# Kernel optimization log

Hardware: AMD Instinct MI355X
Metric: run time of the kernel (lower is better)

Reference implementation:

```python
import jax, jax.numpy as jnp
import numpy as np

B, T, N, U = 64, 128, 128, 128  # batch, seq_len, n_features, lstm units


def setup_inputs() -> dict:
    key = jax.random.key(0)
    ks = jax.random.split(key, 8)
    s = 0.05
    return {
        "x": jax.random.normal(ks[0], (B, T, N), dtype=jnp.float32),
        "hidden_state": jnp.zeros((B, U), jnp.float32),
        "cell_state": jnp.zeros((B, U), jnp.float32),
        "lstm_kernel": jax.random.normal(ks[1], (N, 4 * U), jnp.float32) * s,
        "lstm_bias": jnp.zeros((4 * U,), jnp.float32),
        "w1_kernel": jax.random.normal(ks[2], (1, T), jnp.float32) * s,
        "w1_bias": jnp.zeros((T,), jnp.float32),
        "w2_kernel": jax.random.normal(ks[3], (2 * U, T), jnp.float32) * s,
        "w2_bias": jnp.zeros((T,), jnp.float32),
        "v_kernel": jax.random.normal(ks[4], (T, 1), jnp.float32) * s,
        "v_bias": jnp.zeros((1,), jnp.float32),
        "n": N,
    }


def reference(x, hidden_state, cell_state, lstm_kernel, lstm_bias,
              w1_kernel, w1_bias, w2_kernel, w2_bias, v_kernel, v_bias, n):
    # NewLSTM ignores the provided initial state, so every timestep's LSTM
    # runs a length-1 sequence from zero (h, c). No recurrence -> vectorize
    # over time. Keras gate order: i, f, c(g), o; recurrent kernel * 0 drops out.
    z = x @ lstm_kernel + lstm_bias                       # (B,T,4U)
    i, f, g, o = jnp.split(z, 4, axis=-1)
    c = jax.nn.sigmoid(i) * jnp.tanh(g)                   # f-gate * c_prev(=0) vanishes
    h = jax.nn.sigmoid(o) * jnp.tanh(c)                   # (B,T,U)

    # Input attention per timestep, vectorized over T.
    query = jnp.concatenate([h, c], axis=-1)              # (B,T,2U)
    s2 = query @ w2_kernel + w2_bias                      # (B,T,T)
    # w1 is Dense(T) on a size-1 feature axis: x_scalar * w1_kernel[0] + b.
    s1 = x[..., None] * w1_kernel[0] + w1_bias            # (B,T,N,T)
    score = jnp.tanh(s1 + s2[:, :, None, :])              # (B,T,N,T)
    e = jnp.einsum('btnk,k->btn', score, v_kernel[:, 0]) + v_bias[0]  # (B,T,N)
    alpha = jax.nn.softmax(e, axis=-1)                    # softmax over features

    return x * alpha                                      # (B,T,N)
```

## Files before the change

kernel.cpp:

```cpp
#include <hip/hip_runtime.h>
#include <math.h>


typedef __attribute__((ext_vector_type(8))) short short8;
typedef __attribute__((ext_vector_type(4))) float f32x4;

#define BT 8192
#define NF 128
#define K_C     2.8853900817779268f
#define K_LOG2E 1.4426950408889634f

__device__ __forceinline__ float fast_rcp(float x)  { return __builtin_amdgcn_rcpf(x); }
__device__ __forceinline__ float fast_exp2(float x) { return __builtin_amdgcn_exp2f(x); }

__device__ __forceinline__ float tanh_nc(float tC) {
    return fmaf(-2.f, fast_rcp(1.f + fast_exp2(tC)), 1.f);
}
__device__ __forceinline__ float tanh_fast(float t) { return tanh_nc(t * K_C); }
__device__ __forceinline__ float sig_fast(float z) {
    return fast_rcp(1.f + fast_exp2(-K_LOG2E * z));
}
__device__ __forceinline__ unsigned short f2bf(float f) {
    unsigned u = __float_as_uint(f);
    return (unsigned short)((u + 0x7fffu + ((u >> 16) & 1u)) >> 16);
}

__global__ __launch_bounds__(64) void prep(const float* __restrict__ Wl,
                                           const float* __restrict__ w2,
                                           unsigned short* __restrict__ wsB) {
    const int lane = threadIdx.x;
    const int n16 = lane & 15, q = lane >> 4;
    const int b = blockIdx.x;
    if (b < 96) {
        const int nt = b >> 2, kk = b & 3;
        const int g = nt >> 3, jt = nt & 7;
        const int goff = (g == 0) ? 0 : (g == 1 ? 256 : 384);
        const int col = goff + jt * 16 + n16;
        unsigned short* d = wsB + b * 512 + lane * 8;
        #pragma unroll
        for (int j = 0; j < 8; j++)
            d[j] = f2bf(Wl[(kk * 32 + q * 8 + j) * 512 + col]);
    } else {
        const int fs = b - 96;
        const int nt2 = fs >> 3, kk2 = fs & 7;
        const int col = nt2 * 16 + n16;
        unsigned short* d = wsB + 49152 + fs * 512 + lane * 8;
        #pragma unroll
        for (int j = 0; j < 8; j++)
            d[j] = f2bf(w2[(kk2 * 32 + q * 8 + j) * 128 + col]);
    }
}

__global__ __launch_bounds__(256, 2) void enc(
    const float* __restrict__ x,  const unsigned short* __restrict__ wsB,
    const float* __restrict__ bl, const float* __restrict__ b2,
    const float* __restrict__ b1, const float* __restrict__ w1,
    const float* __restrict__ v,  float* __restrict__ out)
{
    __shared__ __align__(16) float xs[16][NF];
    __shared__ unsigned short Qf[8 * 512];
    __shared__ __align__(16) float c2[16][NF];
    __shared__ __align__(16) float w1Cs[NF], vs[NF];
    __shared__ float Ftab[16][32];
    __shared__ float rowMn[16], rowMx[16];

    const int t    = threadIdx.x;
    const int lane = t & 63, w = t >> 6;
    const int n16  = lane & 15, q = lane >> 4;
    const int rowbase = blockIdx.x * 16;

    for (int i = t; i < 512; i += 256)
        ((float4*)xs)[i] = ((const float4*)(x + rowbase * NF))[i];
    if (t < NF) { w1Cs[t] = w1[t] * K_C; vs[t] = v[t]; }

    short8 af[4];
    const float* xrow = x + (rowbase + n16) * NF + q * 8;
    #pragma unroll
    for (int kk = 0; kk < 4; kk++) {
        const float4 v0 = *(const float4*)(xrow + kk * 32);
        const float4 v1 = *(const float4*)(xrow + kk * 32 + 4);
        short8 a;
        a[0] = f2bf(v0.x); a[1] = f2bf(v0.y); a[2] = f2bf(v0.z); a[3] = f2bf(v0.w);
        a[4] = f2bf(v1.x); a[5] = f2bf(v1.y); a[6] = f2bf(v1.z); a[7] = f2bf(v1.w);
        af[kk] = a;
    }

    f32x4 acc[2][3];
    #pragma unroll
    for (int j2 = 0; j2 < 2; j2++)
        #pragma unroll
        for (int g = 0; g < 3; g++) acc[j2][g] = (f32x4)(0.f);
    const short8* B1g = (const short8*)wsB;
    #pragma unroll
    for (int kk = 0; kk < 4; kk++)
        #pragma unroll
        for (int j2 = 0; j2 < 2; j2++) {
            const int jt = w * 2 + j2;
            #pragma unroll
            for (int g = 0; g < 3; g++) {
                const short8 bf = B1g[(((g * 8 + jt) * 4) + kk) * 64 + lane];
                acc[j2][g] = __builtin_amdgcn_mfma_f32_16x16x32_bf16(
                    af[kk], bf, acc[j2][g], 0, 0, 0);
            }
        }

    #pragma unroll
    for (int j2 = 0; j2 < 2; j2++) {
        const int jt = w * 2 + j2;
        const int u  = jt * 16 + n16;
        const float bi = bl[u], bg = bl[256 + u], bo = bl[384 + u];
        const int kqh = u, kqc = NF + u;
        const int baseh = (kqh >> 5) * 512 + ((kqh & 31) >> 3) * 128 + q * 32 + (kqh & 7);
        const int basec = (kqc >> 5) * 512 + ((kqc & 31) >> 3) * 128 + q * 32 + (kqc & 7);
        #pragma unroll
        for (int r = 0; r < 4; r++) {
            const float c = sig_fast(acc[j2][0][r] + bi) * tanh_fast(acc[j2][1][r] + bg);
            const float h = sig_fast(acc[j2][2][r] + bo) * tanh_fast(c);
            Qf[baseh + r * 8] = f2bf(h);
            Qf[basec + r * 8] = f2bf(c);
        }
    }
    __syncthreads();

    short8 a2[8];
    #pragma unroll
    for (int kk2 = 0; kk2 < 8; kk2++)
        a2[kk2] = *(const short8*)&Qf[kk2 * 512 + lane * 8];
    const short8* B2g = (const short8*)(wsB + 49152);
    #pragma unroll
    for (int j2 = 0; j2 < 2; j2++) {
        const int nt2 = w * 2 + j2;
        f32x4 acc2 = (f32x4)(0.f);
        #pragma unroll
        for (int kk2 = 0; kk2 < 8; kk2++) {
            const short8 bf = B2g[(nt2 * 8 + kk2) * 64 + lane];
            acc2 = __builtin_amdgcn_mfma_f32_16x16x32_bf16(a2[kk2], bf, acc2, 0, 0, 0);
        }
        const int u2 = nt2 * 16 + n16;
        const float bias2 = (b2[u2] + b1[u2]) * K_C;
        #pragma unroll
        for (int r = 0; r < 4; r++)
            c2[q * 4 + r][u2] = fmaf(acc2[r], K_C, bias2);
    }

    #pragma unroll
    for (int r4 = 0; r4 < 4; r4++) {
        const int row = w * 4 + r4;
        float a = xs[row][lane], b = xs[row][64 + lane];
        float mn = fminf(a, b), mx = fmaxf(a, b);
        #pragma unroll
        for (int off = 1; off < 64; off <<= 1) {
            mn = fminf(mn, __shfl_xor(mn, off, 64));
            mx = fmaxf(mx, __shfl_xor(mx, off, 64));
        }
        if (lane == 0) { rowMn[row] = mn; rowMx[row] = mx; }
    }
    __syncthreads();

    #pragma unroll
    for (int p = 0; p < 2; p++) {
        const int row = p * 8 + (t >> 5);
        const int m   = t & 31;
        const float mn = rowMn[row];
        const float h  = (rowMx[row] - mn) * (1.f / 29.f);
        const float xi = fmaf((float)(m - 1), h, mn);
        float accF = 0.f;
        #pragma unroll 4
        for (int k = 0; k < NF; k += 4) {
            const float4 w4 = *(const float4*)&w1Cs[k];
            const float4 c4 = *(const float4*)&c2[row][k];
            const float4 v4 = *(const float4*)&vs[k];
            accF = fmaf(tanh_nc(fmaf(xi, w4.x, c4.x)), v4.x, accF);
            accF = fmaf(tanh_nc(fmaf(xi, w4.y, c4.y)), v4.y, accF);
            accF = fmaf(tanh_nc(fmaf(xi, w4.z, c4.z)), v4.z, accF);
            accF = fmaf(tanh_nc(fmaf(xi, w4.w, c4.w)), v4.w, accF);
        }
        Ftab[row][m] = accF;
    }
    __syncthreads();

    {
        const int row = t >> 4;
        const int n0  = (t & 15) * 8;
        const float mn   = rowMn[row];
        const float span = rowMx[row] - mn;
        const float invh = span > 1e-12f ? 29.f / span : 0.f;
        float xv[8], e8[8];
        *(float4*)&xv[0] = *(const float4*)&xs[row][n0];
        *(float4*)&xv[4] = *(const float4*)&xs[row][n0 + 4];
        #pragma unroll
        for (int i = 0; i < 8; i++) {
            const float sN = fmaf(xv[i] - mn, invh, 1.0f);
            int ii = (int)sN;
            ii = ii < 1 ? 1 : (ii > 29 ? 29 : ii);
            const float f  = sN - (float)ii;
            const float F0 = Ftab[row][ii - 1], F1 = Ftab[row][ii];
            const float F2 = Ftab[row][ii + 1], F3 = Ftab[row][ii + 2];
            e8[i] = F1 + 0.5f * f * ((F2 - F0)
                  + f * ((2.f * F0 - 5.f * F1 + 4.f * F2 - F3)
                  + f * (3.f * (F1 - F2) + F3 - F0)));
        }
        float mval = e8[0];
        #pragma unroll
        for (int i = 1; i < 8; i++) mval = fmaxf(mval, e8[i]);
        #pragma unroll
        for (int off = 1; off < 16; off <<= 1) mval = fmaxf(mval, __shfl_xor(mval, off, 64));
        float ssum = 0.f;
        #pragma unroll
        for (int i = 0; i < 8; i++) { e8[i] = fast_exp2(K_LOG2E * (e8[i] - mval)); ssum += e8[i]; }
        #pragma unroll
        for (int off = 1; off < 16; off <<= 1) ssum += __shfl_xor(ssum, off, 64);
        const float rs = fast_rcp(ssum);
        float4 o0, o1;
        o0.x = xv[0] * e8[0] * rs; o0.y = xv[1] * e8[1] * rs;
        o0.z = xv[2] * e8[2] * rs; o0.w = xv[3] * e8[3] * rs;
        o1.x = xv[4] * e8[4] * rs; o1.y = xv[5] * e8[5] * rs;
        o1.z = xv[6] * e8[6] * rs; o1.w = xv[7] * e8[7] * rs;
        float* op = out + (rowbase + row) * NF + n0;
        *(float4*)op       = o0;
        *(float4*)(op + 4) = o1;
    }
}

extern "C" void kernel_launch(void* const* d_in, const int* in_sizes, int n_in,
                              void* d_out, int out_size, void* d_ws, size_t ws_size,
                              hipStream_t stream) {
    const float* x  = (const float*)d_in[0];
    const float* Wl = (const float*)d_in[3];
    const float* bl = (const float*)d_in[4];
    const float* w1 = (const float*)d_in[5];
    const float* b1 = (const float*)d_in[6];
    const float* w2 = (const float*)d_in[7];
    const float* b2 = (const float*)d_in[8];
    const float* v  = (const float*)d_in[9];
    float* out = (float*)d_out;
    unsigned short* wsB = (unsigned short*)d_ws;

    prep<<<160, 64, 0, stream>>>(Wl, w2, wsB);
    enc<<<BT / 16, 256, 0, stream>>>(x, wsB, bl, b2, b1, w1, v, out);
}
```

Baseline: 94.54 us.

## Use 512-thread blocks, halve interpolation table, load x fragments from LDS

Doubles threads per block so each wave computes a single 16-column MFMA tile, and splits the Ftab build across thread pairs with a shuffle reduction. It reduces the interpolation table from 32 to 16 nodes, halving the tanh evaluations per row at the cost of coarser cubic interpolation accuracy. The row min/max pass is moved ahead of the MFMA phase, x is loaded once into padded shared memory, and the bf16 A fragments are built from there instead of re-reading global memory. An extra barrier is added early on.

```diff
diff --git a/kernel.cpp b/kernel.cpp
--- a/kernel.cpp
+++ b/kernel.cpp
@@ -7,6 +7,7 @@
 
 #define BT 8192
 #define NF 128
+#define XP 132
 #define K_C     2.8853900817779268f
 #define K_LOG2E 1.4426950408889634f
 
@@ -51,17 +52,17 @@
     }
 }
 
-__global__ __launch_bounds__(256, 2) void enc(
+__global__ __launch_bounds__(512, 4) void enc(
     const float* __restrict__ x,  const unsigned short* __restrict__ wsB,
     const float* __restrict__ bl, const float* __restrict__ b2,
     const float* __restrict__ b1, const float* __restrict__ w1,
     const float* __restrict__ v,  float* __restrict__ out)
 {
-    __shared__ __align__(16) float xs[16][NF];
+    __shared__ __align__(16) float xs[16][XP];
     __shared__ unsigned short Qf[8 * 512];
     __shared__ __align__(16) float c2[16][NF];
     __shared__ __align__(16) float w1Cs[NF], vs[NF];
-    __shared__ float Ftab[16][32];
+    __shared__ float Ftab[16][16];
     __shared__ float rowMn[16], rowMx[16];
 
     const int t    = threadIdx.x;
@@ -69,104 +70,94 @@
     const int n16  = lane & 15, q = lane >> 4;
     const int rowbase = blockIdx.x * 16;
 
-    for (int i = t; i < 512; i += 256)
-        ((float4*)xs)[i] = ((const float4*)(x + rowbase * NF))[i];
+    {
+        const int row = t >> 5, c4 = (t & 31) * 4;
+        *(float4*)&xs[row][c4] = *(const float4*)(x + (rowbase + row) * NF + c4);
+    }
     if (t < NF) { w1Cs[t] = w1[t] * K_C; vs[t] = v[t]; }
+    __syncthreads();
+
+    {
+        const int row = t >> 5, c4 = (t & 31) * 4;
+        const float4 xv = *(const float4*)&xs[row][c4];
+        float mn = fminf(fminf(xv.x, xv.y), fminf(xv.z, xv.w));
+        float mx = fmaxf(fmaxf(xv.x, xv.y), fmaxf(xv.z, xv.w));
+        #pragma unroll
+        for (int off = 1; off < 32; off <<= 1) {
+            mn = fminf(mn, __shfl_xor(mn, off, 64));
+            mx = fmaxf(mx, __shfl_xor(mx, off, 64));
+        }
+        if ((t & 31) == 0) { rowMn[row] = mn; rowMx[row] = mx; }
+    }
 
     short8 af[4];
-    const float* xrow = x + (rowbase + n16) * NF + q * 8;
     #pragma unroll
     for (int kk = 0; kk < 4; kk++) {
-        const float4 v0 = *(const float4*)(xrow + kk * 32);
-        const float4 v1 = *(const float4*)(xrow + kk * 32 + 4);
+        const float4 v0 = *(const float4*)&xs[n16][kk * 32 + q * 8];
+        const float4 v1 = *(const float4*)&xs[n16][kk * 32 + q * 8 + 4];
         short8 a;
         a[0] = f2bf(v0.x); a[1] = f2bf(v0.y); a[2] = f2bf(v0.z); a[3] = f2bf(v0.w);
         a[4] = f2bf(v1.x); a[5] = f2bf(v1.y); a[6] = f2bf(v1.z); a[7] = f2bf(v1.w);
         af[kk] = a;
     }
 
-    f32x4 acc[2][3];
+    f32x4 acc[3];
     #pragma unroll
-    for (int j2 = 0; j2 < 2; j2++)
-        #pragma unroll
-        for (int g = 0; g < 3; g++) acc[j2][g] = (f32x4)(0.f);
+    for (int g = 0; g < 3; g++) acc[g] = (f32x4)(0.f);
     const short8* B1g = (const short8*)wsB;
     #pragma unroll
     for (int kk = 0; kk < 4; kk++)
         #pragma unroll
-        for (int j2 = 0; j2 < 2; j2++) {
-            const int jt = w * 2 + j2;
-            #pragma unroll
-            for (int g = 0; g < 3; g++) {
-                const short8 bf = B1g[(((g * 8 + jt) * 4) + kk) * 64 + lane];
-                acc[j2][g] = __builtin_amdgcn_mfma_f32_16x16x32_bf16(
-                    af[kk], bf, acc[j2][g], 0, 0, 0);
-            }
-        }
-
-    #pragma unroll
-    for (int j2 = 0; j2 < 2; j2++) {
-        const int jt = w * 2 + j2;
-        const int u  = jt * 16 + n16;
+        for (int g = 0; g < 3; g++) {
+            const short8 bf = B1g[(((g * 8 + w) * 4) + kk) * 64 + lane];
+            acc[g] = __builtin_amdgcn_mfma_f32_16x16x32_bf16(af[kk], bf, acc[g], 0, 0, 0);
+        }
+
+    const int u = w * 16 + n16;
+    {
         const float bi = bl[u], bg = bl[256 + u], bo = bl[384 + u];
         const int kqh = u, kqc = NF + u;
         const int baseh = (kqh >> 5) * 512 + ((kqh & 31) >> 3) * 128 + q * 32 + (kqh & 7);
         const int basec = (kqc >> 5) * 512 + ((kqc & 31) >> 3) * 128 + q * 32 + (kqc & 7);
         #pragma unroll
         for (int r = 0; r < 4; r++) {
-            const float c = sig_fast(acc[j2][0][r] + bi) * tanh_fast(acc[j2][1][r] + bg);
-            const float h = sig_fast(acc[j2][2][r] + bo) * tanh_fast(c);
+            const float c = sig_fast(acc[0][r] + bi) * tanh_fast(acc[1][r] + bg);
+            const float h = sig_fast(acc[2][r] + bo) * tanh_fast(c);
             Qf[baseh + r * 8] = f2bf(h);
             Qf[basec + r * 8] = f2bf(c);
         }
     }
     __syncthreads();
 
-    short8 a2[8];
-    #pragma unroll
-    for (int kk2 = 0; kk2 < 8; kk2++)
-        a2[kk2] = *(const short8*)&Qf[kk2 * 512 + lane * 8];
-    const short8* B2g = (const short8*)(wsB + 49152);
-    #pragma unroll
-    for (int j2 = 0; j2 < 2; j2++) {
-        const int nt2 = w * 2 + j2;
+    {
+        short8 a2[8];
+        #pragma unroll
+        for (int kk2 = 0; kk2 < 8; kk2++)
+            a2[kk2] = *(const short8*)&Qf[kk2 * 512 + lane * 8];
+        const short8* B2g = (const short8*)(wsB + 49152);
         f32x4 acc2 = (f32x4)(0.f);
         #pragma unroll
         for (int kk2 = 0; kk2 < 8; kk2++) {
-            const short8 bf = B2g[(nt2 * 8 + kk2) * 64 + lane];
+            const short8 bf = B2g[(w * 8 + kk2) * 64 + lane];
             acc2 = __builtin_amdgcn_mfma_f32_16x16x32_bf16(a2[kk2], bf, acc2, 0, 0, 0);
         }
-        const int u2 = nt2 * 16 + n16;
-        const float bias2 = (b2[u2] + b1[u2]) * K_C;
+        const float bias2 = (b2[u] + b1[u]) * K_C;
         #pragma unroll
         for (int r = 0; r < 4; r++)
-            c2[q * 4 + r][u2] = fmaf(acc2[r], K_C, bias2);
-    }
-
-    #pragma unroll
-    for (int r4 = 0; r4 < 4; r4++) {
-        const int row = w * 4 + r4;
-        float a = xs[row][lane], b = xs[row][64 + lane];
-        float mn = fminf(a, b), mx = fmaxf(a, b);
-        #pragma unroll
-        for (int off = 1; off < 64; off <<= 1) {
-            mn = fminf(mn, __shfl_xor(mn, off, 64));
-            mx = fmaxf(mx, __shfl_xor(mx, off, 64));
-        }
-        if (lane == 0) { rowMn[row] = mn; rowMx[row] = mx; }
-    }
-    __syncthreads();
-
-    #pragma unroll
-    for (int p = 0; p < 2; p++) {
-        const int row = p * 8 + (t >> 5);
-        const int m   = t & 31;
+            c2[q * 4 + r][u] = fmaf(acc2[r], K_C, bias2);
+    }
+    __syncthreads();
+
+    {
+        const int row = t >> 5;
+        const int m   = (t >> 1) & 15;
+        const int k0  = (t & 1) * 64;
         const float mn = rowMn[row];
-        const float h  = (rowMx[row] - mn) * (1.f / 29.f);
+        const float h  = (rowMx[row] - mn) * (1.f / 13.f);
         const float xi = fmaf((float)(m - 1), h, mn);
         float accF = 0.f;
         #pragma unroll 4
-        for (int k = 0; k < NF; k += 4) {
+        for (int k = k0; k < k0 + 64; k += 4) {
             const float4 w4 = *(const float4*)&w1Cs[k];
             const float4 c4 = *(const float4*)&c2[row][k];
             const float4 v4 = *(const float4*)&vs[k];
@@ -175,50 +166,50 @@
             accF = fmaf(tanh_nc(fmaf(xi, w4.z, c4.z)), v4.z, accF);
             accF = fmaf(tanh_nc(fmaf(xi, w4.w, c4.w)), v4.w, accF);
         }
-        Ftab[row][m] = accF;
-    }
-    __syncthreads();
-
-    {
-        const int row = t >> 4;
-        const int n0  = (t & 15) * 8;
+        accF += __shfl_xor(accF, 1, 64);
+        if ((t & 1) == 0) Ftab[row][m] = accF;
+    }
+    __syncthreads();
+
+    {
+        const int row = t >> 5;
+        const int n0  = (t & 31) * 4;
         const float mn   = rowMn[row];
         const float span = rowMx[row] - mn;
-        const float invh = span > 1e-12f ? 29.f / span : 0.f;
-        float xv[8], e8[8];
-        *(float4*)&xv[0] = *(const float4*)&xs[row][n0];
-        *(float4*)&xv[4] = *(const float4*)&xs[row][n0 + 4];
-        #pragma unroll
-        for (int i = 0; i < 8; i++) {
-            const float sN = fmaf(xv[i] - mn, invh, 1.0f);
+        const float invh = span > 1e-12f ? 13.f / span : 0.f;
+        const float4 xv = *(const float4*)&xs[row][n0];
+        float xa[4] = {xv.x, xv.y, xv.z, xv.w};
+        float e4[4];
+        #pragma unroll
+        for (int i = 0; i < 4; i++) {
+            const float sN = fmaf(xa[i] - mn, invh, 1.0f);
             int ii = (int)sN;
-            ii = ii < 1 ? 1 : (ii > 29 ? 29 : ii);
+            ii = ii < 1 ? 1 : (ii > 13 ? 13 : ii);
             const float f  = sN - (float)ii;
             const float F0 = Ftab[row][ii - 1], F1 = Ftab[row][ii];
             const float F2 = Ftab[row][ii + 1], F3 = Ftab[row][ii + 2];
-            e8[i] = F1 + 0.5f * f * ((F2 - F0)
+            e4[i] = F1 + 0.5f * f * ((F2 - F0)
                   + f * ((2.f * F0 - 5.f * F1 + 4.f * F2 - F3)
                   + f * (3.f * (F1 - F2) + F3 - F0)));
         }
-        float mval = e8[0];
-        #pragma unroll
-        for (int i = 1; i < 8; i++) mval = fmaxf(mval, e8[i]);
-        #pragma unroll
-        for (int off = 1; off < 16; off <<= 1) mval = fmaxf(mval, __shfl_xor(mval, off, 64));
+        float mval = fmaxf(fmaxf(e4[0], e4[1]), fmaxf(e4[2], e4[3]));
+        #pragma unroll
+        for (int off = 1; off < 32; off <<= 1)
+            mval = fmaxf(mval, __shfl_xor(mval, off, 64));
         float ssum = 0.f;
         #pragma unroll
-        for (int i = 0; i < 8; i++) { e8[i] = fast_exp2(K_LOG2E * (e8[i] - mval)); ssum += e8[i]; }
-        #pragma unroll
-        for (int off = 1; off < 16; off <<= 1) ssum += __shfl_xor(ssum, off, 64);
+        for (int i = 0; i < 4; i++) {
+            e4[i] = fast_exp2(K_LOG2E * (e4[i] - mval));
+            ssum += e4[i];
+        }
+        #pragma unroll
+        for (int off = 1; off < 32; off <<= 1)
+            ssum += __shfl_xor(ssum, off, 64);
         const float rs = fast_rcp(ssum);
-        float4 o0, o1;
-        o0.x = xv[0] * e8[0] * rs; o0.y = xv[1] * e8[1] * rs;
-        o0.z = xv[2] * e8[2] * rs; o0.w = xv[3] * e8[3] * rs;
-        o1.x = xv[4] * e8[4] * rs; o1.y = xv[5] * e8[5] * rs;
-        o1.z = xv[6] * e8[6] * rs; o1.w = xv[7] * e8[7] * rs;
-        float* op = out + (rowbase + row) * NF + n0;
-        *(float4*)op       = o0;
-        *(float4*)(op + 4) = o1;
+        float4 o;
+        o.x = xa[0] * e4[0] * rs; o.y = xa[1] * e4[1] * rs;
+        o.z = xa[2] * e4[2] * rs; o.w = xa[3] * e4[3] * rs;
+        *(float4*)(out + (rowbase + row) * NF + n0) = o;
     }
 }
 
@@ -237,5 +228,5 @@
     unsigned short* wsB = (unsigned short*)d_ws;
 
     prep<<<160, 64, 0, stream>>>(Wl, w2, wsB);
-    enc<<<BT / 16, 256, 0, stream>>>(x, wsB, bl, b2, b1, w1, v, out);
-}
+    enc<<<BT / 16, 512, 0, stream>>>(x, wsB, bl, b2, b1, w1, v, out);
+}
```

Result: faster. 87.93 us (-7.0%).
